# Optimization experiments

Hardware: AMD Instinct MI355X
Metric: run time of the kernel (lower is better)

Reference implementation:

```python
import jax, jax.numpy as jnp
import numpy as np

IN_FEATURES = 16384
OUT_FEATURES = 16384
NNZ = 1_000_000
BATCH = 256


def setup_inputs() -> dict:
    key = jax.random.key(0)
    k1, k2, k3 = jax.random.split(key, 3)
    x = jax.random.normal(k1, (IN_FEATURES, BATCH), dtype=jnp.float32)
    values = jax.random.normal(k2, (NNZ,), dtype=jnp.float32)
    indices = jax.random.randint(k3, (2, NNZ), 0, OUT_FEATURES, dtype=jnp.int64)
    bias = jnp.zeros((OUT_FEATURES, 1), dtype=jnp.float32)
    return {"x": x, "values": values, "indices": indices, "bias": bias}


def reference(x, values, indices, bias):
    # Sparse (COO) matmul: out[r, :] += values[k] * x[c, :] for each nnz (r, c).
    # Equivalent to torch.sparse.mm(W_coo.coalesce(), x) + bias since
    # coalesce() sums duplicate entries and segment_sum does the same.
    row = indices[0]  # [nnz] in [0, OUT_FEATURES)
    col = indices[1]  # [nnz] in [0, IN_FEATURES)
    gathered = values[:, None] * x[col]  # [nnz, B]
    out = jax.ops.segment_sum(gathered, row, num_segments=OUT_FEATURES)  # [out, B]
    return out + bias
```

## Files before the change

### kernel.cpp

```cpp
#include <hip/hip_runtime.h>

typedef unsigned int u32;
typedef unsigned short u16;

constexpr int OUT_F = 16384;
constexpr int IN_F  = 16384;
constexpr int B_N   = 256;
constexpr int NGRP  = 256;
constexpr int GCAP  = 4608;
constexpr int BINB  = 4096;


__global__ __launch_bounds__(1024) void prep_k(
    const int* __restrict__ rows, const int* __restrict__ cols,
    const float* __restrict__ vals, const float* __restrict__ x,
    u16* __restrict__ xb, int* __restrict__ gcnt,
    uint2* __restrict__ gbuck, int nnz, int nbin, int n4) {
  const int tid = threadIdx.x;

  if ((int)blockIdx.x >= nbin) {
    const int i2 = blockIdx.x - nbin;
    for (int j = 0; j < 4; ++j) {
      int k4 = i2 * 4096 + j * 1024 + tid;
      if (k4 < n4) {
        float4 v = ((const float4*)x)[k4];
        u32 u0 = __float_as_uint(v.x), u1 = __float_as_uint(v.y),
            u2 = __float_as_uint(v.z), u3 = __float_as_uint(v.w);
        ushort4 r;
        r.x = (u16)((u0 + 0x7FFFu + ((u0 >> 16) & 1u)) >> 16);
        r.y = (u16)((u1 + 0x7FFFu + ((u1 >> 16) & 1u)) >> 16);
        r.z = (u16)((u2 + 0x7FFFu + ((u2 >> 16) & 1u)) >> 16);
        r.w = (u16)((u3 + 0x7FFFu + ((u3 >> 16) & 1u)) >> 16);
        ((ushort4*)xb)[k4] = r;
      }
    }
    return;
  }

  __shared__ int   hist[NGRP], lofs[NGRP], cur[NGRP], gbase[NGRP], scanb[NGRP];
  __shared__ uint2 stage[BINB];
  __shared__ int   tgt[BINB];

  const int base = blockIdx.x * BINB;
  const int nval = min(BINB, nnz - base);
  if (tid < NGRP) hist[tid] = 0;
  __syncthreads();

  int r[4]; u32 c[4]; float v[4]; bool ok[4];
#pragma unroll
  for (int i = 0; i < 4; ++i) {
    int k = base + i * 1024 + tid;
    ok[i] = k < nnz;
    if (ok[i]) {
      r[i] = rows[k]; c[i] = (u32)cols[k]; v[i] = vals[k];
      atomicAdd(&hist[r[i] >> 6], 1);
    }
  }
  __syncthreads();

  if (tid < NGRP) scanb[tid] = hist[tid];
  __syncthreads();
  for (int off = 1; off < NGRP; off <<= 1) {
    int t = 0;
    if (tid < NGRP && tid >= off) t = scanb[tid - off];
    __syncthreads();
    if (tid < NGRP) scanb[tid] += t;
    __syncthreads();
  }
  if (tid < NGRP) {
    int lo = scanb[tid] - hist[tid];
    lofs[tid] = lo;
    cur[tid]  = lo;
    gbase[tid] = atomicAdd(&gcnt[tid], hist[tid]);
  }
  __syncthreads();

#pragma unroll
  for (int i = 0; i < 4; ++i) {
    if (ok[i]) {
      int g   = r[i] >> 6;
      int pos = atomicAdd(&cur[g], 1);
      stage[pos].x = (c[i] << 6) | (u32)(r[i] & 63);
      stage[pos].y = __float_as_uint(v[i]);
      int w = gbase[g] + (pos - lofs[g]);
      tgt[pos] = (w < GCAP) ? (g * GCAP + w) : -1;
    }
  }
  __syncthreads();

#pragma unroll
  for (int j = 0; j < 4; ++j) {
    int idx = j * 1024 + tid;
    if (idx < nval) {
      int t = tgt[idx];
      if (t >= 0) gbuck[t] = stage[idx];
    }
  }
}

__global__ __launch_bounds__(1024) void regroup_k(
    int* __restrict__ gcnt, uint2* __restrict__ gbuck,
    int* __restrict__ rowstart, int* __restrict__ rowcnt) {
  __shared__ int hist[4096];
  __shared__ int part[1024];
  const int tid = threadIdx.x;
  const int g   = blockIdx.x;
  int cnt = gcnt[g];
  if (cnt > GCAP) cnt = GCAP;
  uint2* bk = gbuck + (size_t)g * GCAP;

#pragma unroll
  for (int i = 0; i < 4; ++i) hist[i * 1024 + tid] = 0;
  __syncthreads();

  uint2 e[5]; int bin[5]; bool ok[5];
#pragma unroll
  for (int i = 0; i < 5; ++i) {
    int k = i * 1024 + tid;
    ok[i] = k < cnt;
    if (ok[i]) {
      e[i] = bk[k];
      bin[i] = (int)(((e[i].x & 63u) << 6) | ((e[i].x >> 6) >> 8));
      atomicAdd(&hist[bin[i]], 1);
    }
  }
  __syncthreads();

  int loc[4]; int s = 0;
#pragma unroll
  for (int i = 0; i < 4; ++i) { loc[i] = hist[tid * 4 + i]; s += loc[i]; }
  part[tid] = s;
  __syncthreads();
  for (int off = 1; off < 1024; off <<= 1) {
    int t = (tid >= off) ? part[tid - off] : 0;
    __syncthreads();
    part[tid] += t;
    __syncthreads();
  }
  int run = (tid == 0) ? 0 : part[tid - 1];
  __syncthreads();
#pragma unroll
  for (int i = 0; i < 4; ++i) { hist[tid * 4 + i] = run; run += loc[i]; }
  __syncthreads();

  if (tid < 64) {
    int lo = hist[tid << 6];
    int hi = (tid == 63) ? cnt : hist[(tid + 1) << 6];
    rowstart[g * 64 + tid] = g * GCAP + lo;
    rowcnt[g * 64 + tid]   = hi - lo;
  }
  __syncthreads();

#pragma unroll
  for (int i = 0; i < 5; ++i) {
    if (ok[i]) {
      int pos = atomicAdd(&hist[bin[i]], 1);
      bk[pos] = e[i];
    }
  }
}

__global__ __launch_bounds__(256) void spmm_final_k(
    const int* __restrict__ rowstart, const int* __restrict__ rowcnt,
    const uint2* __restrict__ gbuck, const u16* __restrict__ xb,
    const float* __restrict__ bias, float* __restrict__ out) {
  const int lane = threadIdx.x & 63;
  const int wid  = threadIdx.x >> 6;
  const int r    = blockIdx.x * 4 + wid;
  const int cnt  = rowcnt[r];
  const uint2* bk = gbuck + rowstart[r];
  float a0 = 0.f, a1 = 0.f, a2 = 0.f, a3 = 0.f;
  for (int base = 0; base < cnt; base += 64) {
    const int m = min(64, cnt - base);
    uint2 pk = make_uint2(0u, 0u);
    if (lane < m) pk = bk[base + lane];
    int j = 0;
    for (; j + 4 <= m; j += 4) {
      u32 k0 = (u32)__builtin_amdgcn_readlane((int)pk.x, j);
      u32 v0b = (u32)__builtin_amdgcn_readlane((int)pk.y, j);
      u32 k1 = (u32)__builtin_amdgcn_readlane((int)pk.x, j + 1);
      u32 v1b = (u32)__builtin_amdgcn_readlane((int)pk.y, j + 1);
      u32 k2 = (u32)__builtin_amdgcn_readlane((int)pk.x, j + 2);
      u32 v2b = (u32)__builtin_amdgcn_readlane((int)pk.y, j + 2);
      u32 k3 = (u32)__builtin_amdgcn_readlane((int)pk.x, j + 3);
      u32 v3b = (u32)__builtin_amdgcn_readlane((int)pk.y, j + 3);
      uint2 x0 = ((const uint2*)(xb + ((size_t)(k0 >> 6) << 8)))[lane];
      uint2 x1 = ((const uint2*)(xb + ((size_t)(k1 >> 6) << 8)))[lane];
      uint2 x2 = ((const uint2*)(xb + ((size_t)(k2 >> 6) << 8)))[lane];
      uint2 x3 = ((const uint2*)(xb + ((size_t)(k3 >> 6) << 8)))[lane];
      float v0 = __uint_as_float(v0b), v1 = __uint_as_float(v1b);
      float v2 = __uint_as_float(v2b), v3 = __uint_as_float(v3b);
      a0 = fmaf(v0, __uint_as_float(x0.x << 16), a0);
      a1 = fmaf(v0, __uint_as_float(x0.x & 0xFFFF0000u), a1);
      a2 = fmaf(v0, __uint_as_float(x0.y << 16), a2);
      a3 = fmaf(v0, __uint_as_float(x0.y & 0xFFFF0000u), a3);
      a0 = fmaf(v1, __uint_as_float(x1.x << 16), a0);
      a1 = fmaf(v1, __uint_as_float(x1.x & 0xFFFF0000u), a1);
      a2 = fmaf(v1, __uint_as_float(x1.y << 16), a2);
      a3 = fmaf(v1, __uint_as_float(x1.y & 0xFFFF0000u), a3);
      a0 = fmaf(v2, __uint_as_float(x2.x << 16), a0);
      a1 = fmaf(v2, __uint_as_float(x2.x & 0xFFFF0000u), a1);
      a2 = fmaf(v2, __uint_as_float(x2.y << 16), a2);
      a3 = fmaf(v2, __uint_as_float(x2.y & 0xFFFF0000u), a3);
      a0 = fmaf(v3, __uint_as_float(x3.x << 16), a0);
      a1 = fmaf(v3, __uint_as_float(x3.x & 0xFFFF0000u), a1);
      a2 = fmaf(v3, __uint_as_float(x3.y << 16), a2);
      a3 = fmaf(v3, __uint_as_float(x3.y & 0xFFFF0000u), a3);
    }
    for (; j < m; ++j) {
      u32 kk = (u32)__builtin_amdgcn_readlane((int)pk.x, j);
      u32 vb = (u32)__builtin_amdgcn_readlane((int)pk.y, j);
      float v = __uint_as_float(vb);
      uint2 xx = ((const uint2*)(xb + ((size_t)(kk >> 6) << 8)))[lane];
      a0 = fmaf(v, __uint_as_float(xx.x << 16), a0);
      a1 = fmaf(v, __uint_as_float(xx.x & 0xFFFF0000u), a1);
      a2 = fmaf(v, __uint_as_float(xx.y << 16), a2);
      a3 = fmaf(v, __uint_as_float(xx.y & 0xFFFF0000u), a3);
    }
  }
  const float bv = bias[r];
  float4 o;
  o.x = a0 + bv; o.y = a1 + bv; o.z = a2 + bv; o.w = a3 + bv;
  ((float4*)(out + (size_t)r * B_N))[lane] = o;
}


__global__ __launch_bounds__(256) void hist_k(const int* __restrict__ rows,
                                              int* __restrict__ counts, int nnz) {
  int k = blockIdx.x * 256 + threadIdx.x;
  if (k < nnz) atomicAdd(&counts[rows[k]], 1);
}

__global__ __launch_bounds__(1024) void scan_k(const int* __restrict__ counts,
                                               int* __restrict__ offsets,
                                               int* __restrict__ cursor) {
  __shared__ int part[1024];
  const int tid  = threadIdx.x;
  const int base = tid * 16;
  int loc[16];
  int s = 0;
#pragma unroll
  for (int i = 0; i < 16; ++i) { loc[i] = counts[base + i]; s += loc[i]; }
  part[tid] = s;
  __syncthreads();
  for (int off = 1; off < 1024; off <<= 1) {
    int v = (tid >= off) ? part[tid - off] : 0;
    __syncthreads();
    part[tid] += v;
    __syncthreads();
  }
  int run = (tid == 0) ? 0 : part[tid - 1];
#pragma unroll
  for (int i = 0; i < 16; ++i) {
    offsets[base + i] = run;
    cursor[base + i]  = run;
    run += loc[i];
  }
  if (tid == 1023) offsets[OUT_F] = run;
}

__global__ __launch_bounds__(256) void scatter_k(const int* __restrict__ rows,
                                                 const int* __restrict__ colsIn,
                                                 const float* __restrict__ vals,
                                                 int* __restrict__ cursor,
                                                 int* __restrict__ colsOut,
                                                 float* __restrict__ valsOut,
                                                 int nnz) {
  int k = blockIdx.x * 256 + threadIdx.x;
  if (k < nnz) {
    int r   = rows[k];
    int pos = atomicAdd(&cursor[r], 1);
    colsOut[pos] = colsIn[k];
    valsOut[pos] = vals[k];
  }
}

__global__ __launch_bounds__(256) void spmm_k(const int* __restrict__ offsets,
                                              const int* __restrict__ cols,
                                              const float* __restrict__ vals,
                                              const float* __restrict__ x,
                                              const float* __restrict__ bias,
                                              float* __restrict__ out) {
  __shared__ int   c_lds[256];
  __shared__ float v_lds[256];
  const int r = blockIdx.x;
  const int b = threadIdx.x;
  const int start = offsets[r];
  const int end   = offsets[r + 1];
  float acc = 0.f;
  for (int basei = start; basei < end; basei += 256) {
    const int n = min(256, end - basei);
    if (threadIdx.x < n) {
      c_lds[threadIdx.x] = cols[basei + threadIdx.x];
      v_lds[threadIdx.x] = vals[basei + threadIdx.x];
    }
    __syncthreads();
    for (int j = 0; j < n; ++j) {
      acc = fmaf(v_lds[j], x[(size_t)c_lds[j] * B_N + b], acc);
    }
    __syncthreads();
  }
  out[(size_t)r * B_N + b] = acc + bias[r];
}


__global__ __launch_bounds__(256) void initout_k(const float* __restrict__ bias,
                                                 float* __restrict__ out) {
  int i = blockIdx.x * 256 + threadIdx.x;
  out[i] = bias[i >> 8];
}

__global__ __launch_bounds__(256) void atomic_k(const int* __restrict__ rows,
                                                const int* __restrict__ colsIn,
                                                const float* __restrict__ vals,
                                                const float* __restrict__ x,
                                                float* __restrict__ out, int nnz) {
  int k = blockIdx.x;
  if (k < nnz) {
    int r = rows[k], c = colsIn[k];
    float v = vals[k];
    int b = threadIdx.x;
    atomicAdd(&out[(size_t)r * B_N + b], v * x[(size_t)c * B_N + b]);
  }
}

extern "C" void kernel_launch(void* const* d_in, const int* in_sizes, int n_in,
                              void* d_out, int out_size, void* d_ws, size_t ws_size,
                              hipStream_t stream) {
  const float* x      = (const float*)d_in[0];
  const float* values = (const float*)d_in[1];
  const int*   idx    = (const int*)d_in[2];
  const float* bias   = (const float*)d_in[3];
  float* out = (float*)d_out;

  const int nnz = in_sizes[2] / 2;
  const int* rows   = idx;
  const int* colsIn = idx + nnz;

  char* ws = (char*)d_ws;
  auto align256 = [](size_t v) { return (v + 255) & ~(size_t)255; };

  size_t t1_gcnt  = 0;
  size_t t1_rs    = align256(t1_gcnt + (size_t)NGRP * 4);
  size_t t1_rc    = align256(t1_rs + (size_t)OUT_F * 4);
  size_t t1_gbuck = align256(t1_rc + (size_t)OUT_F * 4);
  size_t t1_xb    = align256(t1_gbuck + (size_t)NGRP * GCAP * 8);
  size_t t1_need  = align256(t1_xb + (size_t)IN_F * B_N * 2);

  size_t t2_counts  = 0;
  size_t t2_offsets = align256(t2_counts + (size_t)OUT_F * 4);
  size_t t2_cursor  = align256(t2_offsets + ((size_t)OUT_F + 1) * 4);
  size_t t2_cols    = align256(t2_cursor + (size_t)OUT_F * 4);
  size_t t2_vals    = align256(t2_cols + (size_t)nnz * 4);
  size_t t2_need    = align256(t2_vals + (size_t)nnz * 4);

  if (ws_size >= t1_need) {
    int*   gcnt     = (int*)(ws + t1_gcnt);
    int*   rowstart = (int*)(ws + t1_rs);
    int*   rowcnt   = (int*)(ws + t1_rc);
    uint2* gbuck    = (uint2*)(ws + t1_gbuck);
    u16*   xb       = (u16*)(ws + t1_xb);

    const int n4   = IN_F * B_N / 4;
    const int nbin = (nnz + BINB - 1) / BINB;
    const int nxc  = (n4 + 4095) / 4096;

    hipMemsetAsync(gcnt, 0, (size_t)NGRP * 4, stream);
    prep_k<<<nbin + nxc, 1024, 0, stream>>>(rows, colsIn, values, x, xb, gcnt,
                                            gbuck, nnz, nbin, n4);
    regroup_k<<<NGRP, 1024, 0, stream>>>(gcnt, gbuck, rowstart, rowcnt);
    spmm_final_k<<<OUT_F / 4, 256, 0, stream>>>(rowstart, rowcnt, gbuck, xb,
                                                bias, out);
  } else if (ws_size >= t2_need) {
    int*   counts  = (int*)(ws + t2_counts);
    int*   offsets = (int*)(ws + t2_offsets);
    int*   cursor  = (int*)(ws + t2_cursor);
    int*   colsB   = (int*)(ws + t2_cols);
    float* valsB   = (float*)(ws + t2_vals);

    const int nblk = (nnz + 255) / 256;
    hipMemsetAsync(counts, 0, (size_t)OUT_F * 4, stream);
    hist_k<<<nblk, 256, 0, stream>>>(rows, counts, nnz);
    scan_k<<<1, 1024, 0, stream>>>(counts, offsets, cursor);
    scatter_k<<<nblk, 256, 0, stream>>>(rows, colsIn, values, cursor, colsB, valsB, nnz);
    spmm_k<<<OUT_F, 256, 0, stream>>>(offsets, colsB, valsB, x, bias, out);
  } else {
    initout_k<<<(out_size + 255) / 256, 256, 0, stream>>>(bias, out);
    atomic_k<<<nnz, 256, 0, stream>>>(rows, colsIn, values, x, out, nnz);
  }
}
```

Before: 76.21 us.

## Split SpMM into four column-window passes for gather locality

Regroup now records four column-window boundaries per row instead of a start and count. The SpMM runs as four launches, one per column quarter. The first pass writes accumulations plus bias, and later passes read-modify-write the output. The aim is to shrink the working set of gathered x rows per pass so it stays cache-resident. In exchange it adds three extra read-modify-write passes over the output and more kernel launches.

```diff
diff --git a/kernel.cpp b/kernel.cpp
--- a/kernel.cpp
+++ b/kernel.cpp
@@ -100,7 +100,7 @@
 
 __global__ __launch_bounds__(1024) void regroup_k(
     int* __restrict__ gcnt, uint2* __restrict__ gbuck,
-    int* __restrict__ rowstart, int* __restrict__ rowcnt) {
+    int4* __restrict__ rowwin, int* __restrict__ rowend) {
   __shared__ int hist[4096];
   __shared__ int part[1024];
   const int tid = threadIdx.x;
@@ -144,10 +144,14 @@
   __syncthreads();
 
   if (tid < 64) {
-    int lo = hist[tid << 6];
-    int hi = (tid == 63) ? cnt : hist[(tid + 1) << 6];
-    rowstart[g * 64 + tid] = g * GCAP + lo;
-    rowcnt[g * 64 + tid]   = hi - lo;
+    const int gb = g * GCAP;
+    int4 w;
+    w.x = gb + hist[(tid << 6)];
+    w.y = gb + hist[(tid << 6) + 16];
+    w.z = gb + hist[(tid << 6) + 32];
+    w.w = gb + hist[(tid << 6) + 48];
+    rowwin[g * 64 + tid] = w;
+    rowend[g * 64 + tid] = gb + ((tid == 63) ? cnt : hist[(tid + 1) << 6]);
   }
   __syncthreads();
 
@@ -160,15 +164,22 @@
   }
 }
 
-__global__ __launch_bounds__(256) void spmm_final_k(
-    const int* __restrict__ rowstart, const int* __restrict__ rowcnt,
+template <int P>
+__global__ __launch_bounds__(256) void spmm_win_k(
+    const int4* __restrict__ rowwin, const int* __restrict__ rowend,
     const uint2* __restrict__ gbuck, const u16* __restrict__ xb,
     const float* __restrict__ bias, float* __restrict__ out) {
   const int lane = threadIdx.x & 63;
   const int wid  = threadIdx.x >> 6;
   const int r    = blockIdx.x * 4 + wid;
-  const int cnt  = rowcnt[r];
-  const uint2* bk = gbuck + rowstart[r];
+  const int4 w4  = rowwin[r];
+  int s, e;
+  if constexpr (P == 0)      { s = w4.x; e = w4.y; }
+  else if constexpr (P == 1) { s = w4.y; e = w4.z; }
+  else if constexpr (P == 2) { s = w4.z; e = w4.w; }
+  else                       { s = w4.w; e = rowend[r]; }
+  const int cnt   = e - s;
+  const uint2* bk = gbuck + s;
   float a0 = 0.f, a1 = 0.f, a2 = 0.f, a3 = 0.f;
   for (int base = 0; base < cnt; base += 64) {
     const int m = min(64, cnt - base);
@@ -218,10 +229,16 @@
       a3 = fmaf(v, __uint_as_float(xx.y & 0xFFFF0000u), a3);
     }
   }
-  const float bv = bias[r];
+  float4* dst = (float4*)(out + (size_t)r * B_N) + lane;
   float4 o;
-  o.x = a0 + bv; o.y = a1 + bv; o.z = a2 + bv; o.w = a3 + bv;
-  ((float4*)(out + (size_t)r * B_N))[lane] = o;
+  if constexpr (P == 0) {
+    const float bv = bias[r];
+    o.x = a0 + bv; o.y = a1 + bv; o.z = a2 + bv; o.w = a3 + bv;
+  } else {
+    float4 prev = *dst;
+    o.x = prev.x + a0; o.y = prev.y + a1; o.z = prev.z + a2; o.w = prev.w + a3;
+  }
+  *dst = o;
 }
 
 
@@ -341,9 +358,9 @@
   auto align256 = [](size_t v) { return (v + 255) & ~(size_t)255; };
 
   size_t t1_gcnt  = 0;
-  size_t t1_rs    = align256(t1_gcnt + (size_t)NGRP * 4);
-  size_t t1_rc    = align256(t1_rs + (size_t)OUT_F * 4);
-  size_t t1_gbuck = align256(t1_rc + (size_t)OUT_F * 4);
+  size_t t1_rw    = align256(t1_gcnt + (size_t)NGRP * 4);
+  size_t t1_re    = align256(t1_rw + (size_t)OUT_F * 16);
+  size_t t1_gbuck = align256(t1_re + (size_t)OUT_F * 4);
   size_t t1_xb    = align256(t1_gbuck + (size_t)NGRP * GCAP * 8);
   size_t t1_need  = align256(t1_xb + (size_t)IN_F * B_N * 2);
 
@@ -355,11 +372,11 @@
   size_t t2_need    = align256(t2_vals + (size_t)nnz * 4);
 
   if (ws_size >= t1_need) {
-    int*   gcnt     = (int*)(ws + t1_gcnt);
-    int*   rowstart = (int*)(ws + t1_rs);
-    int*   rowcnt   = (int*)(ws + t1_rc);
-    uint2* gbuck    = (uint2*)(ws + t1_gbuck);
-    u16*   xb       = (u16*)(ws + t1_xb);
+    int*   gcnt   = (int*)(ws + t1_gcnt);
+    int4*  rowwin = (int4*)(ws + t1_rw);
+    int*   rowend = (int*)(ws + t1_re);
+    uint2* gbuck  = (uint2*)(ws + t1_gbuck);
+    u16*   xb     = (u16*)(ws + t1_xb);
 
     const int n4   = IN_F * B_N / 4;
     const int nbin = (nnz + BINB - 1) / BINB;
@@ -368,9 +385,11 @@
     hipMemsetAsync(gcnt, 0, (size_t)NGRP * 4, stream);
     prep_k<<<nbin + nxc, 1024, 0, stream>>>(rows, colsIn, values, x, xb, gcnt,
                                             gbuck, nnz, nbin, n4);
-    regroup_k<<<NGRP, 1024, 0, stream>>>(gcnt, gbuck, rowstart, rowcnt);
-    spmm_final_k<<<OUT_F / 4, 256, 0, stream>>>(rowstart, rowcnt, gbuck, xb,
-                                                bias, out);
+    regroup_k<<<NGRP, 1024, 0, stream>>>(gcnt, gbuck, rowwin, rowend);
+    spmm_win_k<0><<<OUT_F / 4, 256, 0, stream>>>(rowwin, rowend, gbuck, xb, bias, out);
+    spmm_win_k<1><<<OUT_F / 4, 256, 0, stream>>>(rowwin, rowend, gbuck, xb, bias, out);
+    spmm_win_k<2><<<OUT_F / 4, 256, 0, stream>>>(rowwin, rowend, gbuck, xb, bias, out);
+    spmm_win_k<3><<<OUT_F / 4, 256, 0, stream>>>(rowwin, rowend, gbuck, xb, bias, out);
   } else if (ws_size >= t2_need) {
     int*   counts  = (int*)(ws + t2_counts);
     int*   offsets = (int*)(ws + t2_offsets);
```

After: 89.14 us. +17.0%, slower.
